# Kernel tuning notes

Hardware: AMD Instinct MI355X
Metric: run time of the kernel (lower is better)

The kernel has to match this reference:

```python
import jax, jax.numpy as jnp
import numpy as np

N, E = 100000, 1600000
IN, HID, NCLS = 128, 128, 64


def setup_inputs() -> dict:
    key = jax.random.key(0)
    ks = jax.random.split(key, 8)
    x = jax.random.normal(ks[0], (N, IN), jnp.float32)
    edge_index = jax.random.randint(ks[1], (2, E), 0, N, dtype=jnp.int32)
    s1 = 1.0 / np.sqrt(IN)
    s2 = 1.0 / np.sqrt(HID)
    return {
        "x": x,
        "edge_index": edge_index,
        "Wl1": jax.random.uniform(ks[2], (IN, HID), jnp.float32, -s1, s1),
        "Wr1": jax.random.uniform(ks[3], (IN, HID), jnp.float32, -s1, s1),
        "b1": jnp.zeros((HID,), jnp.float32),
        "Wl2": jax.random.uniform(ks[4], (HID, NCLS), jnp.float32, -s2, s2),
        "Wr2": jax.random.uniform(ks[5], (HID, NCLS), jnp.float32, -s2, s2),
        "b2": jnp.zeros((NCLS,), jnp.float32),
    }


def _sage_conv(x, src, dst, inv_deg, Wl, Wr, b):
    # mean-aggregate neighbor features at each destination node (PyG SAGEConv)
    agg = jax.ops.segment_sum(x[src], dst, num_segments=N)  # [N, d]
    agg = agg * inv_deg[:, None]
    # out = lin_l(mean_j x_j) + lin_r(x_i); bias lives in lin_l
    return agg @ Wl + x @ Wr + b


def reference(x, edge_index, Wl1, Wr1, b1, Wl2, Wr2, b2):
    src, dst = edge_index[0], edge_index[1]
    deg = jax.ops.segment_sum(jnp.ones((E,), jnp.float32), dst, num_segments=N)
    inv_deg = 1.0 / jnp.maximum(deg, 1.0)
    h = _sage_conv(x, src, dst, inv_deg, Wl1, Wr1, b1)
    h = jax.nn.relu(h)
    # dropout is identity at inference (training=False)
    h = _sage_conv(h, src, dst, inv_deg, Wl2, Wr2, b2)
    return jax.nn.log_softmax(h, axis=1)
```

## Files before the change

### kernel.cpp

```cpp
#include <hip/hip_runtime.h>
#include <hip/hip_bf16.h>


typedef __attribute__((ext_vector_type(8))) short short8;
typedef __attribute__((ext_vector_type(4))) float f32x4;
typedef __attribute__((ext_vector_type(2))) float f32x2;

#define NPB 512
#define BCAP 16384
#define CHUNK 8192

__device__ __forceinline__ ushort f2bf(float f) {
    unsigned u = __float_as_uint(f);
    return (ushort)((u + 0x7fff + ((u >> 16) & 1)) >> 16);
}
__device__ __forceinline__ float bflo(unsigned v) { return __uint_as_float(v << 16); }
__device__ __forceinline__ float bfhi(unsigned v) { return __uint_as_float(v & 0xffff0000u); }
__device__ __forceinline__ unsigned pk4bf(float a, float b) {
    return (unsigned)f2bf(a) | ((unsigned)f2bf(b) << 16);
}
__device__ __forceinline__ f32x2 shflx2(f32x2 v, int m) {
    f32x2 r; r[0] = __shfl_xor(v[0], m); r[1] = __shfl_xor(v[1], m); return r;
}

__device__ __forceinline__ void wfrag_one(const float* W, ushort* Wf, int i, int COLS) {
    int j = i & 7, m = (i >> 3) & 15, kc = (i >> 7) & 15, ct = i >> 11;
    Wf[i] = f2bf(W[(kc * 8 + j) * COLS + ct * 16 + m]);
}

__global__ void __launch_bounds__(256)
k1_scatter_cvtw(const int* __restrict__ src, const int* __restrict__ dst,
                int* __restrict__ bcount, unsigned* __restrict__ bbuf, int E, int NSC,
                const float* __restrict__ Wl1, const float* __restrict__ Wr1,
                const float* __restrict__ Wl2, const float* __restrict__ Wr2,
                ushort* __restrict__ Wf_l1, ushort* __restrict__ Wf_r1,
                ushort* __restrict__ Wf_l2, ushort* __restrict__ Wf_r2) {
    int tid = threadIdx.x;
    if ((int)blockIdx.x >= NSC) {
        int i = ((int)blockIdx.x - NSC) * 256 + tid;
        if (i < 16384)       wfrag_one(Wl1, Wf_l1, i, 128);
        else if (i < 32768)  wfrag_one(Wr1, Wf_r1, i - 16384, 128);
        else if (i < 40960)  wfrag_one(Wl2, Wf_l2, i - 32768, 64);
        else if (i < 49152)  wfrag_one(Wr2, Wf_r2, i - 40960, 64);
        return;
    }
    __shared__ unsigned entry[CHUNK];
    __shared__ unsigned char ebkt[CHUNK];
    __shared__ int lhist[256], lbase[256], lcur[256];
    lhist[tid] = 0;
    __syncthreads();
    int e0 = blockIdx.x * CHUNK;
    int cnt = min(CHUNK, E - e0);
    int nv = cnt >> 2;
    for (int t = tid; t < nv; t += 256) {
        int4 d4 = ((const int4*)(dst + e0))[t];
        int4 s4 = ((const int4*)(src + e0))[t];
        int i = t * 4;
        int b0 = d4.x >> 9, b1 = d4.y >> 9, b2 = d4.z >> 9, b3 = d4.w >> 9;
        entry[i + 0] = ((unsigned)s4.x << 9) | (unsigned)(d4.x & 511);
        entry[i + 1] = ((unsigned)s4.y << 9) | (unsigned)(d4.y & 511);
        entry[i + 2] = ((unsigned)s4.z << 9) | (unsigned)(d4.z & 511);
        entry[i + 3] = ((unsigned)s4.w << 9) | (unsigned)(d4.w & 511);
        ebkt[i + 0] = (unsigned char)b0; ebkt[i + 1] = (unsigned char)b1;
        ebkt[i + 2] = (unsigned char)b2; ebkt[i + 3] = (unsigned char)b3;
        atomicAdd(&lhist[b0], 1); atomicAdd(&lhist[b1], 1);
        atomicAdd(&lhist[b2], 1); atomicAdd(&lhist[b3], 1);
    }
    for (int i = (nv << 2) + tid; i < cnt; i += 256) {
        int d = dst[e0 + i], s = src[e0 + i];
        int b = d >> 9;
        entry[i] = ((unsigned)s << 9) | (unsigned)(d & 511);
        ebkt[i] = (unsigned char)b;
        atomicAdd(&lhist[b], 1);
    }
    __syncthreads();
    int h = lhist[tid];
    lbase[tid] = (h > 0) ? atomicAdd(&bcount[tid], h) : 0;
    lcur[tid] = 0;
    __syncthreads();
    for (int i = tid; i < cnt; i += 256) {
        int b = ebkt[i];
        int o = atomicAdd(&lcur[b], 1);
        bbuf[(long)b * BCAP + lbase[b] + o] = entry[i];
    }
}

template <int COLS, bool F32IN>
__device__ __forceinline__ void proj_body(int bid, int tid,
                            const void* __restrict__ xin,
                            const ushort* __restrict__ Wfl, const ushort* __restrict__ Wfr,
                            const float* __restrict__ bias,
                            unsigned char* __restrict__ p8, ushort* __restrict__ q, int N) {
    constexpr int CT = COLS / 16;
    int wave = tid >> 6, lane = tid & 63;
    int quad = lane >> 4, m = lane & 15;
    long row0 = (long)bid * 64 + wave * 16;
    long node = row0 + m;
    long arow = (node < N) ? node : (N - 1);

    f32x4 accp[CT], accq[CT];
#pragma unroll
    for (int ct = 0; ct < CT; ++ct) { accp[ct] = (f32x4)0.0f; accq[ct] = (f32x4)0.0f; }

#pragma unroll
    for (int kk = 0; kk < 128; kk += 32) {
        short8 b;
        if (F32IN) {
            const float* xf = (const float*)xin + arow * 128 + kk + quad * 8;
            float4 f0 = *(const float4*)xf;
            float4 f1 = *(const float4*)(xf + 4);
            b[0] = (short)f2bf(f0.x); b[1] = (short)f2bf(f0.y);
            b[2] = (short)f2bf(f0.z); b[3] = (short)f2bf(f0.w);
            b[4] = (short)f2bf(f1.x); b[5] = (short)f2bf(f1.y);
            b[6] = (short)f2bf(f1.z); b[7] = (short)f2bf(f1.w);
        } else {
            b = *(const short8*)((const ushort*)xin + arow * 128 + kk + quad * 8);
        }
        int kc = (kk >> 3) + quad;
#pragma unroll
        for (int ct = 0; ct < CT; ++ct) {
            long boff = (((long)(ct * 16 + kc) * 16) + m) * 8;
            short8 al = *(const short8*)(Wfl + boff);
            short8 ar = *(const short8*)(Wfr + boff);
            accp[ct] = __builtin_amdgcn_mfma_f32_16x16x32_bf16(al, b, accp[ct], 0, 0, 0);
            accq[ct] = __builtin_amdgcn_mfma_f32_16x16x32_bf16(ar, b, accq[ct], 0, 0, 0);
        }
    }

    if (node < N) {
#pragma unroll
        for (int ct = 0; ct < CT; ++ct) {
            int c0 = ct * 16 + quad * 4;
            float4 bv = *(const float4*)(bias + c0);
            float q0 = accq[ct][0] + bv.x, q1 = accq[ct][1] + bv.y;
            float q2 = accq[ct][2] + bv.z, q3 = accq[ct][3] + bv.w;
            unsigned w = (unsigned)__builtin_amdgcn_cvt_pk_fp8_f32(accp[ct][0], accp[ct][1], 0, false);
            w = (unsigned)__builtin_amdgcn_cvt_pk_fp8_f32(accp[ct][2], accp[ct][3], (int)w, true);
            *(unsigned*)(p8 + node * COLS + c0) = w;
            uint2 qw; qw.x = pk4bf(q0, q1); qw.y = pk4bf(q2, q3);
            *(uint2*)(q + node * COLS + c0) = qw;
        }
    }
}

__global__ void __launch_bounds__(256)
k2_csr_proj1(const unsigned* __restrict__ bbuf, const int* __restrict__ bcount,
             int* __restrict__ row_start, int* __restrict__ degw,
             float* __restrict__ inv_deg, int* __restrict__ ssrc, int NBcsr, int N,
             const float* __restrict__ x,
             const ushort* __restrict__ Wfl, const ushort* __restrict__ Wfr,
             const float* __restrict__ bias,
             unsigned char* __restrict__ p8, ushort* __restrict__ q) {
    int tid = threadIdx.x;
    if ((int)blockIdx.x >= NBcsr) {
        proj_body<128, true>((int)blockIdx.x - NBcsr, tid, x, Wfl, Wfr, bias, p8, q, N);
        return;
    }
    __shared__ int sdeg[NPB], lcur[NPB];
    int b = blockIdx.x;
    int node0 = b * NPB;
    sdeg[tid] = 0; sdeg[tid + 256] = 0;
    __syncthreads();
    int cnt = bcount[b];
    long base = (long)b * BCAP;
    for (int i = tid; i < cnt; i += 256)
        atomicAdd(&sdeg[bbuf[base + i] & 511], 1);
    __syncthreads();
    int c0 = sdeg[tid], c1 = sdeg[tid + 256];
    for (int off = 1; off < NPB; off <<= 1) {
        int a0 = (tid >= off) ? sdeg[tid - off] : 0;
        int a1 = (tid + 256 >= off) ? sdeg[tid + 256 - off] : 0;
        __syncthreads();
        sdeg[tid] += a0; sdeg[tid + 256] += a1;
        __syncthreads();
    }
    int rs0 = sdeg[tid] - c0;
    int rs1 = sdeg[tid + 256] - c1;
    lcur[tid] = rs0; lcur[tid + 256] = rs1;
    if (node0 + tid < N) {
        row_start[node0 + tid] = (int)(base + rs0);
        degw[node0 + tid] = c0;
        inv_deg[node0 + tid] = 1.0f / (float)(c0 > 1 ? c0 : 1);
    }
    if (node0 + tid + 256 < N) {
        row_start[node0 + tid + 256] = (int)(base + rs1);
        degw[node0 + tid + 256] = c1;
        inv_deg[node0 + tid + 256] = 1.0f / (float)(c1 > 1 ? c1 : 1);
    }
    __syncthreads();
    for (int i = tid; i < cnt; i += 256) {
        unsigned w = bbuf[base + i];
        int pos = atomicAdd(&lcur[w & 511], 1);
        ssrc[base + pos] = (int)(w >> 9);
    }
}

__global__ void __launch_bounds__(256)
agg_relu_kernel(const unsigned char* __restrict__ p8,
                const ushort* __restrict__ q,
                const int* __restrict__ ssrc,
                const int* __restrict__ row_start,
                const int* __restrict__ deg,
                const float* __restrict__ inv_deg,
                ushort* __restrict__ hb, int N) {
    int wave = threadIdx.x >> 6, lane = threadIdx.x & 63;
    int n = blockIdx.x * 4 + wave;
    if (n >= N) return;
    int g = lane >> 4, lm = lane & 15;
    int start = row_start[n], d = deg[n];
    const int* sp = ssrc + start;
    const unsigned char* pb = p8 + lm * 8;
    f32x2 a0 = (f32x2)0.f, a1 = (f32x2)0.f, a2 = (f32x2)0.f, a3 = (f32x2)0.f;
    int j = 0;
    for (; j + 16 <= d; j += 16) {
        int s0 = sp[j + g], s1 = sp[j + 4 + g], s2 = sp[j + 8 + g], s3 = sp[j + 12 + g];
        uint2 v0 = *(const uint2*)(pb + (long)s0 * 128);
        uint2 v1 = *(const uint2*)(pb + (long)s1 * 128);
        uint2 v2 = *(const uint2*)(pb + (long)s2 * 128);
        uint2 v3 = *(const uint2*)(pb + (long)s3 * 128);
#pragma unroll
        for (int t = 0; t < 4; ++t) {
            uint2 vv = (t == 0) ? v0 : (t == 1) ? v1 : (t == 2) ? v2 : v3;
            a0 += __builtin_amdgcn_cvt_pk_f32_fp8((int)vv.x, false);
            a1 += __builtin_amdgcn_cvt_pk_f32_fp8((int)vv.x, true);
            a2 += __builtin_amdgcn_cvt_pk_f32_fp8((int)vv.y, false);
            a3 += __builtin_amdgcn_cvt_pk_f32_fp8((int)vv.y, true);
        }
    }
    for (; j < d; j += 4) {
        int idx = j + g;
        int s = sp[idx < d ? idx : j];
        uint2 vv = *(const uint2*)(pb + (long)s * 128);
        if (idx < d) {
            a0 += __builtin_amdgcn_cvt_pk_f32_fp8((int)vv.x, false);
            a1 += __builtin_amdgcn_cvt_pk_f32_fp8((int)vv.x, true);
            a2 += __builtin_amdgcn_cvt_pk_f32_fp8((int)vv.y, false);
            a3 += __builtin_amdgcn_cvt_pk_f32_fp8((int)vv.y, true);
        }
    }
    a0 += shflx2(a0, 16); a1 += shflx2(a1, 16);
    a2 += shflx2(a2, 16); a3 += shflx2(a3, 16);
    a0 += shflx2(a0, 32); a1 += shflx2(a1, 32);
    a2 += shflx2(a2, 32); a3 += shflx2(a3, 32);
    if (g == 0) {
        float iv = inv_deg[n];
        uint4 qv = *(const uint4*)(q + (long)n * 128 + lm * 8);
        float h0 = fmaxf(a0[0] * iv + bflo(qv.x), 0.f);
        float h1 = fmaxf(a0[1] * iv + bfhi(qv.x), 0.f);
        float h2 = fmaxf(a1[0] * iv + bflo(qv.y), 0.f);
        float h3 = fmaxf(a1[1] * iv + bfhi(qv.y), 0.f);
        float h4 = fmaxf(a2[0] * iv + bflo(qv.z), 0.f);
        float h5 = fmaxf(a2[1] * iv + bfhi(qv.z), 0.f);
        float h6 = fmaxf(a3[0] * iv + bflo(qv.w), 0.f);
        float h7 = fmaxf(a3[1] * iv + bfhi(qv.w), 0.f);
        uint4 hw;
        hw.x = pk4bf(h0, h1); hw.y = pk4bf(h2, h3);
        hw.z = pk4bf(h4, h5); hw.w = pk4bf(h6, h7);
        *(uint4*)(hb + (long)n * 128 + lm * 8) = hw;
    }
}

__global__ void __launch_bounds__(256)
proj2_kernel(const ushort* __restrict__ hb,
             const ushort* __restrict__ Wfl, const ushort* __restrict__ Wfr,
             const float* __restrict__ bias,
             unsigned char* __restrict__ u8, ushort* __restrict__ v, int N) {
    proj_body<64, false>((int)blockIdx.x, (int)threadIdx.x, hb, Wfl, Wfr, bias, u8, v, N);
}

__global__ void __launch_bounds__(256)
agg_lsm_kernel(const unsigned char* __restrict__ u8,
               const ushort* __restrict__ v,
               const int* __restrict__ ssrc,
               const int* __restrict__ row_start,
               const int* __restrict__ deg,
               const float* __restrict__ inv_deg,
               float* __restrict__ out, int N) {
    int wave = threadIdx.x >> 6, lane = threadIdx.x & 63;
    int n = blockIdx.x * 4 + wave;
    if (n >= N) return;
    int g = lane >> 3, lm = lane & 7;
    int start = row_start[n], d = deg[n];
    const int* sp = ssrc + start;
    const unsigned char* ub = u8 + lm * 8;
    f32x2 a0 = (f32x2)0.f, a1 = (f32x2)0.f, a2 = (f32x2)0.f, a3 = (f32x2)0.f;
    int j = 0;
    for (; j + 16 <= d; j += 16) {
        int s0 = sp[j + g], s1 = sp[j + 8 + g];
        uint2 v0 = *(const uint2*)(ub + (long)s0 * 64);
        uint2 v1 = *(const uint2*)(ub + (long)s1 * 64);
#pragma unroll
        for (int t = 0; t < 2; ++t) {
            uint2 vv = (t == 0) ? v0 : v1;
            a0 += __builtin_amdgcn_cvt_pk_f32_fp8((int)vv.x, false);
            a1 += __builtin_amdgcn_cvt_pk_f32_fp8((int)vv.x, true);
            a2 += __builtin_amdgcn_cvt_pk_f32_fp8((int)vv.y, false);
            a3 += __builtin_amdgcn_cvt_pk_f32_fp8((int)vv.y, true);
        }
    }
    for (; j < d; j += 8) {
        int idx = j + g;
        int s = sp[idx < d ? idx : j];
        uint2 vv = *(const uint2*)(ub + (long)s * 64);
        if (idx < d) {
            a0 += __builtin_amdgcn_cvt_pk_f32_fp8((int)vv.x, false);
            a1 += __builtin_amdgcn_cvt_pk_f32_fp8((int)vv.x, true);
            a2 += __builtin_amdgcn_cvt_pk_f32_fp8((int)vv.y, false);
            a3 += __builtin_amdgcn_cvt_pk_f32_fp8((int)vv.y, true);
        }
    }
    a0 += shflx2(a0, 8);  a1 += shflx2(a1, 8);  a2 += shflx2(a2, 8);  a3 += shflx2(a3, 8);
    a0 += shflx2(a0, 16); a1 += shflx2(a1, 16); a2 += shflx2(a2, 16); a3 += shflx2(a3, 16);
    a0 += shflx2(a0, 32); a1 += shflx2(a1, 32); a2 += shflx2(a2, 32); a3 += shflx2(a3, 32);

    float iv = inv_deg[n];
    uint4 vv = *(const uint4*)(v + (long)n * 64 + lm * 8);
    float z0 = a0[0] * iv + bflo(vv.x), z1 = a0[1] * iv + bfhi(vv.x);
    float z2 = a1[0] * iv + bflo(vv.y), z3 = a1[1] * iv + bfhi(vv.y);
    float z4 = a2[0] * iv + bflo(vv.z), z5 = a2[1] * iv + bfhi(vv.z);
    float z6 = a3[0] * iv + bflo(vv.w), z7 = a3[1] * iv + bfhi(vv.w);
    float mx = fmaxf(fmaxf(fmaxf(z0, z1), fmaxf(z2, z3)),
                     fmaxf(fmaxf(z4, z5), fmaxf(z6, z7)));
#pragma unroll
    for (int o = 4; o > 0; o >>= 1) mx = fmaxf(mx, __shfl_xor(mx, o));
    float e = (__expf(z0 - mx) + __expf(z1 - mx)) + (__expf(z2 - mx) + __expf(z3 - mx)) +
              (__expf(z4 - mx) + __expf(z5 - mx)) + (__expf(z6 - mx) + __expf(z7 - mx));
#pragma unroll
    for (int o = 4; o > 0; o >>= 1) e += __shfl_xor(e, o);
    float ls = mx + __logf(e);
    if (g == 0) {
        float4 o0, o1;
        o0.x = z0 - ls; o0.y = z1 - ls; o0.z = z2 - ls; o0.w = z3 - ls;
        o1.x = z4 - ls; o1.y = z5 - ls; o1.z = z6 - ls; o1.w = z7 - ls;
        *(float4*)(out + (long)n * 64 + lm * 8) = o0;
        *(float4*)(out + (long)n * 64 + lm * 8 + 4) = o1;
    }
}

extern "C" void kernel_launch(void* const* d_in, const int* in_sizes, int n_in,
                              void* d_out, int out_size, void* d_ws, size_t ws_size,
                              hipStream_t stream) {
    const float* x   = (const float*)d_in[0];
    const int*   ei  = (const int*)d_in[1];
    const float* Wl1 = (const float*)d_in[2];
    const float* Wr1 = (const float*)d_in[3];
    const float* b1  = (const float*)d_in[4];
    const float* Wl2 = (const float*)d_in[5];
    const float* Wr2 = (const float*)d_in[6];
    const float* b2  = (const float*)d_in[7];

    const int N = in_sizes[0] / 128;
    const int E = in_sizes[1] / 2;
    const int* src = ei;
    const int* dst = ei + E;
    const int NB = (N + NPB - 1) / NPB;
    const int NSC = (E + CHUNK - 1) / CHUNK;

    size_t off = 0;
    auto take = [&](size_t nbytes) -> void* {
        void* ptr = (void*)((char*)d_ws + off);
        off += (nbytes + 255) & ~(size_t)255;
        return ptr;
    };
    int*      bcount    = (int*)take((size_t)NB * 4);
    unsigned* bbuf      = (unsigned*)take((size_t)NB * BCAP * 4);
    int*      row_start = (int*)take((size_t)N * 4);
    int*      degw      = (int*)take((size_t)N * 4);
    float*    inv_deg   = (float*)take((size_t)N * 4);
    int*      ssrc      = (int*)take((size_t)NB * BCAP * 4);
    unsigned char* p8   = (unsigned char*)take((size_t)N * 128);
    ushort*   q         = (ushort*)take((size_t)N * 128 * 2);
    ushort*   hb        = (ushort*)take((size_t)N * 128 * 2);
    ushort*   Wf_l1     = (ushort*)take(128 * 128 * 2);
    ushort*   Wf_r1     = (ushort*)take(128 * 128 * 2);
    ushort*   Wf_l2     = (ushort*)take(64 * 128 * 2);
    ushort*   Wf_r2     = (ushort*)take(64 * 128 * 2);
    unsigned char* u8 = p8;
    ushort*        v  = q;
    (void)ws_size; (void)n_in; (void)out_size;

    hipMemsetAsync(bcount, 0, (size_t)NB * 4, stream);

    k1_scatter_cvtw<<<NSC + 192, 256, 0, stream>>>(src, dst, bcount, bbuf, E, NSC,
                                                   Wl1, Wr1, Wl2, Wr2,
                                                   Wf_l1, Wf_r1, Wf_l2, Wf_r2);

    int P1 = (N + 63) / 64;
    k2_csr_proj1<<<NB + P1, 256, 0, stream>>>(bbuf, bcount, row_start, degw, inv_deg,
                                              ssrc, NB, N, x, Wf_l1, Wf_r1, b1, p8, q);

    agg_relu_kernel<<<(N + 3) / 4, 256, 0, stream>>>(p8, q, ssrc, row_start, degw, inv_deg, hb, N);

    proj2_kernel<<<(N + 63) / 64, 256, 0, stream>>>(hb, Wf_l2, Wf_r2, b2, u8, v, N);
    agg_lsm_kernel<<<(N + 3) / 4, 256, 0, stream>>>(u8, v, ssrc, row_start, degw, inv_deg,
                                                    (float*)d_out, N);
}
```

Baseline: 285.3 us.

## Stage projection weights in LDS and widen proj/CSR blocks to 512 threads

The projection kernels now copy both bf16 weight matrices into shared memory once per block and read MFMA operands from LDS instead of global memory. Blocks grow to 512 threads covering 128 nodes, so the staged weights serve twice as many rows. The CSR build part is rewritten for 512 threads with one node per thread, vectorized uint4 edge reads, and a wave-shuffle prefix scan in place of the barrier-heavy shared-memory scan. The cost is 64KB of dynamic shared memory per block for the first layer's projection, which limits how many blocks fit on a CU, plus a staging copy and extra barrier at the start of every block.

Result: faster. 260.4 us (-8.7%).

```diff
diff --git a/kernel.cpp b/kernel.cpp
--- a/kernel.cpp
+++ b/kernel.cpp
@@ -85,16 +85,36 @@
     }
 }
 
+template <int CTOT>
+__device__ __forceinline__ void stage_weights(const ushort* __restrict__ Wfl,
+                                              const ushort* __restrict__ Wfr,
+                                              ushort* dst, int tid) {
+    constexpr int HALF = CTOT / 2;
+    constexpr int ITERS = (CTOT * 2) / 8192;
+#pragma unroll
+    for (int r = 0; r < ITERS; ++r) {
+        int u = r * 4096 + tid * 8;
+        const ushort* s = (u < HALF) ? (Wfl + u) : (Wfr + (u - HALF));
+        *(short8*)(dst + u) = *(const short8*)s;
+    }
+}
+
 template <int COLS, bool F32IN>
 __device__ __forceinline__ void proj_body(int bid, int tid,
                             const void* __restrict__ xin,
                             const ushort* __restrict__ Wfl, const ushort* __restrict__ Wfr,
                             const float* __restrict__ bias,
-                            unsigned char* __restrict__ p8, ushort* __restrict__ q, int N) {
+                            unsigned char* __restrict__ p8, ushort* __restrict__ q, int N,
+                            ushort* wsm) {
     constexpr int CT = COLS / 16;
+    stage_weights<2 * COLS * 128>(Wfl, Wfr, wsm, tid);
+    __syncthreads();
+    const ushort* Wl = wsm;
+    const ushort* Wr = wsm + COLS * 128;
+
     int wave = tid >> 6, lane = tid & 63;
     int quad = lane >> 4, m = lane & 15;
-    long row0 = (long)bid * 64 + wave * 16;
+    long row0 = (long)bid * 128 + wave * 16;
     long node = row0 + m;
     long arow = (node < N) ? node : (N - 1);
 
@@ -119,9 +139,9 @@
         int kc = (kk >> 3) + quad;
 #pragma unroll
         for (int ct = 0; ct < CT; ++ct) {
-            long boff = (((long)(ct * 16 + kc) * 16) + m) * 8;
-            short8 al = *(const short8*)(Wfl + boff);
-            short8 ar = *(const short8*)(Wfr + boff);
+            int boff = ((ct * 16 + kc) * 16 + m) * 8;
+            short8 al = *(const short8*)(Wl + boff);
+            short8 ar = *(const short8*)(Wr + boff);
             accp[ct] = __builtin_amdgcn_mfma_f32_16x16x32_bf16(al, b, accp[ct], 0, 0, 0);
             accq[ct] = __builtin_amdgcn_mfma_f32_16x16x32_bf16(ar, b, accq[ct], 0, 0, 0);
         }
@@ -143,7 +163,7 @@
     }
 }
 
-__global__ void __launch_bounds__(256)
+__global__ void __launch_bounds__(512, 4)
 k2_csr_proj1(const unsigned* __restrict__ bbuf, const int* __restrict__ bcount,
              int* __restrict__ row_start, int* __restrict__ degw,
              float* __restrict__ inv_deg, int* __restrict__ ssrc, int NBcsr, int N,
@@ -151,45 +171,67 @@
              const ushort* __restrict__ Wfl, const ushort* __restrict__ Wfr,
              const float* __restrict__ bias,
              unsigned char* __restrict__ p8, ushort* __restrict__ q) {
+    extern __shared__ char smem[];
     int tid = threadIdx.x;
     if ((int)blockIdx.x >= NBcsr) {
-        proj_body<128, true>((int)blockIdx.x - NBcsr, tid, x, Wfl, Wfr, bias, p8, q, N);
+        proj_body<128, true>((int)blockIdx.x - NBcsr, tid, x, Wfl, Wfr, bias, p8, q, N,
+                             (ushort*)smem);
         return;
     }
-    __shared__ int sdeg[NPB], lcur[NPB];
+    int* sdeg = (int*)smem;
+    int* lcur = sdeg + NPB;
+    int* wsum = lcur + NPB;
     int b = blockIdx.x;
     int node0 = b * NPB;
-    sdeg[tid] = 0; sdeg[tid + 256] = 0;
+    sdeg[tid] = 0;
     __syncthreads();
     int cnt = bcount[b];
     long base = (long)b * BCAP;
-    for (int i = tid; i < cnt; i += 256)
-        atomicAdd(&sdeg[bbuf[base + i] & 511], 1);
-    __syncthreads();
-    int c0 = sdeg[tid], c1 = sdeg[tid + 256];
-    for (int off = 1; off < NPB; off <<= 1) {
-        int a0 = (tid >= off) ? sdeg[tid - off] : 0;
-        int a1 = (tid + 256 >= off) ? sdeg[tid + 256 - off] : 0;
-        __syncthreads();
-        sdeg[tid] += a0; sdeg[tid + 256] += a1;
-        __syncthreads();
-    }
-    int rs0 = sdeg[tid] - c0;
-    int rs1 = sdeg[tid + 256] - c1;
-    lcur[tid] = rs0; lcur[tid + 256] = rs1;
+    const unsigned* bb = bbuf + base;
+    int nv = cnt >> 2;
+    for (int t = tid; t < nv; t += 512) {
+        uint4 e = ((const uint4*)bb)[t];
+        atomicAdd(&sdeg[e.x & 511], 1);
+        atomicAdd(&sdeg[e.y & 511], 1);
+        atomicAdd(&sdeg[e.z & 511], 1);
+        atomicAdd(&sdeg[e.w & 511], 1);
+    }
+    for (int i = (nv << 2) + tid; i < cnt; i += 512)
+        atomicAdd(&sdeg[bb[i] & 511], 1);
+    __syncthreads();
+    int lane = tid & 63, wv = tid >> 6;
+    int c0 = sdeg[tid];
+    int v = c0;
+#pragma unroll
+    for (int o = 1; o < 64; o <<= 1) {
+        int t = __shfl_up(v, o);
+        if (lane >= o) v += t;
+    }
+    if (lane == 63) wsum[wv] = v;
+    __syncthreads();
+    int add = 0;
+    for (int w = 0; w < wv; ++w) add += wsum[w];
+    int rs0 = v + add - c0;
+    lcur[tid] = rs0;
     if (node0 + tid < N) {
         row_start[node0 + tid] = (int)(base + rs0);
         degw[node0 + tid] = c0;
         inv_deg[node0 + tid] = 1.0f / (float)(c0 > 1 ? c0 : 1);
     }
-    if (node0 + tid + 256 < N) {
-        row_start[node0 + tid + 256] = (int)(base + rs1);
-        degw[node0 + tid + 256] = c1;
-        inv_deg[node0 + tid + 256] = 1.0f / (float)(c1 > 1 ? c1 : 1);
-    }
-    __syncthreads();
-    for (int i = tid; i < cnt; i += 256) {
-        unsigned w = bbuf[base + i];
+    __syncthreads();
+    for (int t = tid; t < nv; t += 512) {
+        uint4 e = ((const uint4*)bb)[t];
+        int p0 = atomicAdd(&lcur[e.x & 511], 1);
+        int p1 = atomicAdd(&lcur[e.y & 511], 1);
+        int p2 = atomicAdd(&lcur[e.z & 511], 1);
+        int p3 = atomicAdd(&lcur[e.w & 511], 1);
+        ssrc[base + p0] = (int)(e.x >> 9);
+        ssrc[base + p1] = (int)(e.y >> 9);
+        ssrc[base + p2] = (int)(e.z >> 9);
+        ssrc[base + p3] = (int)(e.w >> 9);
+    }
+    for (int i = (nv << 2) + tid; i < cnt; i += 512) {
+        unsigned w = bb[i];
         int pos = atomicAdd(&lcur[w & 511], 1);
         ssrc[base + pos] = (int)(w >> 9);
     }
@@ -260,12 +302,14 @@
     }
 }
 
-__global__ void __launch_bounds__(256)
+__global__ void __launch_bounds__(512, 4)
 proj2_kernel(const ushort* __restrict__ hb,
              const ushort* __restrict__ Wfl, const ushort* __restrict__ Wfr,
              const float* __restrict__ bias,
              unsigned char* __restrict__ u8, ushort* __restrict__ v, int N) {
-    proj_body<64, false>((int)blockIdx.x, (int)threadIdx.x, hb, Wfl, Wfr, bias, u8, v, N);
+    __shared__ ushort wsm[2 * 64 * 128];
+    proj_body<64, false>((int)blockIdx.x, (int)threadIdx.x, hb, Wfl, Wfr, bias, u8, v, N,
+                         wsm);
 }
 
 __global__ void __launch_bounds__(256)
@@ -379,19 +423,26 @@
     ushort*        v  = q;
     (void)ws_size; (void)n_in; (void)out_size;
 
+    static bool attr_set = false;
+    if (!attr_set) {
+        hipFuncSetAttribute((const void*)k2_csr_proj1,
+                            hipFuncAttributeMaxDynamicSharedMemorySize, 65536);
+        attr_set = true;
+    }
+
     hipMemsetAsync(bcount, 0, (size_t)NB * 4, stream);
 
     k1_scatter_cvtw<<<NSC + 192, 256, 0, stream>>>(src, dst, bcount, bbuf, E, NSC,
                                                    Wl1, Wr1, Wl2, Wr2,
                                                    Wf_l1, Wf_r1, Wf_l2, Wf_r2);
 
-    int P1 = (N + 63) / 64;
-    k2_csr_proj1<<<NB + P1, 256, 0, stream>>>(bbuf, bcount, row_start, degw, inv_deg,
-                                              ssrc, NB, N, x, Wf_l1, Wf_r1, b1, p8, q);
+    int P1 = (N + 127) / 128;
+    k2_csr_proj1<<<NB + P1, 512, 65536, stream>>>(bbuf, bcount, row_start, degw, inv_deg,
+                                                  ssrc, NB, N, x, Wf_l1, Wf_r1, b1, p8, q);
 
     agg_relu_kernel<<<(N + 3) / 4, 256, 0, stream>>>(p8, q, ssrc, row_start, degw, inv_deg, hb, N);
 
-    proj2_kernel<<<(N + 63) / 64, 256, 0, stream>>>(hb, Wf_l2, Wf_r2, b2, u8, v, N);
+    proj2_kernel<<<(N + 127) / 128, 512, 0, stream>>>(hb, Wf_l2, Wf_r2, b2, u8, v, N);
     agg_lsm_kernel<<<(N + 3) / 4, 256, 0, stream>>>(u8, v, ssrc, row_start, degw, inv_deg,
                                                     (float*)d_out, N);
 }
```
